# Optimization experiments

Hardware: AMD Instinct MI355X
Metric: run time of the kernel (lower is better)

Reference implementation:

```python
import jax, jax.numpy as jnp
import numpy as np

B, S, IN, OUT = 4, 2048, 4096, 4096


def setup_inputs() -> dict:
    key = jax.random.key(0)
    kx, kw, kb = jax.random.split(key, 3)
    x = jax.random.randint(kx, (B, S, IN), -127, 128, dtype=jnp.int8)
    weight = jax.random.randint(kw, (OUT, IN), -127, 128, dtype=jnp.int8)
    # original module initializes bias to zeros(int32); use random int32 to exercise the add
    bias = jax.random.randint(kb, (1, OUT), -1000, 1000, dtype=jnp.int32)
    return {"x": x, "weight": weight, "bias": bias}


def reference(x, weight, bias):
    x_shape = x.shape
    x2 = x.reshape(-1, x_shape[-1])  # [tokens, IN], int8
    # dot_general with preferred_element_type=int32 -> int8 inputs, int32 accumulate
    y = jax.lax.dot_general(
        x2, weight,
        dimension_numbers=(((1,), (1,)), ((), ())),
        preferred_element_type=jnp.int32,
    )  # [tokens, OUT] int32
    y = y + bias  # broadcast [1, OUT] int32
    return y.reshape(*x_shape[:-1], -1)
```

## Files before the change

kernel.cpp:

```cpp
#include <hip/hip_runtime.h>
#include <stdint.h>

#define M_TOT 8192
#define N_TOT 4096
#define K_TOT 4096

typedef int v4i  __attribute__((ext_vector_type(4)));
typedef int v16i __attribute__((ext_vector_type(16)));

__device__ __forceinline__ void gload_lds16(const void* g, void* l) {
    __builtin_amdgcn_global_load_lds(
        (const __attribute__((address_space(1))) unsigned int*)g,
        (__attribute__((address_space(3))) unsigned int*)l,
        16, 0, 0);
}

#define WAIT_VMCNT0() __builtin_amdgcn_s_waitcnt(0x0f70)

__global__ __launch_bounds__(256) void pack_i32_to_i8(
        const int4* __restrict__ src, int* __restrict__ dst, int n4) {
    int idx = blockIdx.x * 1024 + threadIdx.x;
#pragma unroll
    for (int u = 0; u < 4; ++u, idx += 256) {
        const int4 a = src[idx];
        dst[idx] = (a.x & 255) | ((a.y & 255) << 8) |
                   ((a.z & 255) << 16) | (a.w << 24);
    }
}

__global__ __launch_bounds__(256, 1) void i8gemm_bias(
        const signed char* __restrict__ x,
        const signed char* __restrict__ w,
        const int* __restrict__ bias,
        int* __restrict__ out) {
    __shared__ __align__(16) signed char la[2][256 * 64];
    __shared__ __align__(16) signed char lb[2][256 * 64];

    const int tid  = threadIdx.x;
    const int lane = tid & 63;
    const int wv   = tid >> 6;
    const int l31  = lane & 31;
    const int kh   = lane >> 5;
    const int wr   = wv >> 1;
    const int wc   = wv & 1;

    const int flat = blockIdx.y * gridDim.x + blockIdx.x;
    const int swz  = (flat & 7) * 64 + (flat >> 3);
    const int bn0  = (swz & 15) * 256;
    const int bm0  = (swz >> 4) * 256;

    int bv[4];
#pragma unroll
    for (int j = 0; j < 4; ++j) bv[j] = bias[bn0 + wc * 128 + j * 32 + l31];
    v16i acc[4][4];
#pragma unroll
    for (int i = 0; i < 4; ++i)
#pragma unroll
        for (int j = 0; j < 4; ++j)
#pragma unroll
            for (int r = 0; r < 16; ++r) acc[i][j][r] = bv[j];

    const int fc = (lane & 3) ^ ((lane >> 3) & 3);
    const signed char* pa = x + (long)(bm0 + wv * 64 + (lane >> 2)) * K_TOT + fc * 16;
    const signed char* pb = w + (long)(bn0 + wv * 64 + (lane >> 2)) * K_TOT + fc * 16;
    const int lbase = wv * 64 * 64;

    const int swr = (l31 >> 1) & 3;

#pragma unroll
    for (int i = 0; i < 4; ++i) {
        gload_lds16(pa + (long)i * 16 * K_TOT, &la[0][lbase + i * 1024]);
        gload_lds16(pb + (long)i * 16 * K_TOT, &lb[0][lbase + i * 1024]);
    }

    for (int kt = 0; kt < K_TOT / 64; ++kt) {
        const int cur = kt & 1;
        const signed char* lac = la[cur];
        const signed char* lbc = lb[cur];

        WAIT_VMCNT0();
        __builtin_amdgcn_s_barrier();
        __builtin_amdgcn_sched_barrier(0);

        v4i af[2][4], bf[2][4];
#pragma unroll
        for (int kk = 0; kk < 2; ++kk) {
            const int cs = ((kk * 2 + kh) ^ swr) * 16;
#pragma unroll
            for (int i = 0; i < 4; ++i) {
                af[kk][i] = *(const v4i*)(lac + (wr * 128 + i * 32 + l31) * 64 + cs);
                bf[kk][i] = *(const v4i*)(lbc + (wc * 128 + i * 32 + l31) * 64 + cs);
            }
        }
        __builtin_amdgcn_sched_barrier(0);

        if (kt + 1 < K_TOT / 64) {
            const long k0 = (long)(kt + 1) * 64;
            signed char* lan = la[cur ^ 1] + lbase;
            signed char* lbn = lb[cur ^ 1] + lbase;
#pragma unroll
            for (int i = 0; i < 4; ++i) {
                gload_lds16(pa + k0 + (long)i * 16 * K_TOT, lan + i * 1024);
                gload_lds16(pb + k0 + (long)i * 16 * K_TOT, lbn + i * 1024);
            }
        }
        __builtin_amdgcn_sched_barrier(0);

#pragma unroll
        for (int kk = 0; kk < 2; ++kk)
#pragma unroll
            for (int i = 0; i < 4; ++i)
#pragma unroll
                for (int j = 0; j < 4; ++j)
                    acc[i][j] = __builtin_amdgcn_mfma_i32_32x32x32_i8(
                        af[kk][i], bf[kk][j], acc[i][j], 0, 0, 0);
    }

#pragma unroll
    for (int i = 0; i < 4; ++i) {
        const int mbase = bm0 + wr * 128 + i * 32 + 4 * kh;
#pragma unroll
        for (int j = 0; j < 4; ++j) {
            const int n = bn0 + wc * 128 + j * 32 + l31;
#pragma unroll
            for (int r = 0; r < 16; ++r) {
                const int m = mbase + (r & 3) + 8 * (r >> 2);
                out[(long)m * N_TOT + n] = acc[i][j][r];
            }
        }
    }
}

extern "C" void kernel_launch(void* const* d_in, const int* in_sizes, int n_in,
                              void* d_out, int out_size, void* d_ws, size_t ws_size,
                              hipStream_t stream) {
    const int* x32  = (const int*)d_in[0];
    const int* w32  = (const int*)d_in[1];
    const int* bias = (const int*)d_in[2];
    int*       out  = (int*)d_out;

    signed char* xp = (signed char*)d_ws;
    signed char* wp = (signed char*)d_ws + (size_t)M_TOT * K_TOT;

    const int n4x = (M_TOT * K_TOT) / 4;
    const int n4w = (N_TOT * K_TOT) / 4;
    pack_i32_to_i8<<<n4x / 1024, 256, 0, stream>>>((const int4*)x32, (int*)xp, n4x);
    pack_i32_to_i8<<<n4w / 1024, 256, 0, stream>>>((const int4*)w32, (int*)wp, n4w);

    dim3 grid(N_TOT / 256, M_TOT / 256);
    i8gemm_bias<<<grid, 256, 0, stream>>>(xp, wp, bias, out);
}
```

Before: 418.0 us.

## Triple-buffer LDS tiles and prefetch two K-steps ahead in int8 GEMM

Replaces the double-buffered LDS pipeline with three rotating buffers per operand. Each iteration issues global-to-LDS loads for tile kt+2 and waits only until at most 8 loads are outstanding, instead of draining all of them. This gives global loads about a full extra iteration to arrive, so memory latency hides better behind the MFMA work. The cost is LDS growing from 64KB to 96KB and the pointer rotation adding some address arithmetic.

```diff
diff --git a/kernel.cpp b/kernel.cpp
--- a/kernel.cpp
+++ b/kernel.cpp
@@ -16,6 +16,7 @@
 }
 
 #define WAIT_VMCNT0() __builtin_amdgcn_s_waitcnt(0x0f70)
+#define WAIT_VMCNT8() __builtin_amdgcn_s_waitcnt(0x0f78)
 
 __global__ __launch_bounds__(256) void pack_i32_to_i8(
         const int4* __restrict__ src, int* __restrict__ dst, int n4) {
@@ -33,8 +34,8 @@
         const signed char* __restrict__ w,
         const int* __restrict__ bias,
         int* __restrict__ out) {
-    __shared__ __align__(16) signed char la[2][256 * 64];
-    __shared__ __align__(16) signed char lb[2][256 * 64];
+    __shared__ __align__(16) signed char la[3][256 * 64];
+    __shared__ __align__(16) signed char lb[3][256 * 64];
 
     const int tid  = threadIdx.x;
     const int lane = tid & 63;
@@ -67,19 +68,34 @@
 
     const int swr = (l31 >> 1) & 3;
 
+    signed char* A0 = &la[0][0]; signed char* A1 = &la[1][0]; signed char* A2 = &la[2][0];
+    signed char* B0 = &lb[0][0]; signed char* B1 = &lb[1][0]; signed char* B2 = &lb[2][0];
+
 #pragma unroll
     for (int i = 0; i < 4; ++i) {
-        gload_lds16(pa + (long)i * 16 * K_TOT, &la[0][lbase + i * 1024]);
-        gload_lds16(pb + (long)i * 16 * K_TOT, &lb[0][lbase + i * 1024]);
+        gload_lds16(pa + (long)i * 16 * K_TOT, A0 + lbase + i * 1024);
+        gload_lds16(pb + (long)i * 16 * K_TOT, B0 + lbase + i * 1024);
+    }
+#pragma unroll
+    for (int i = 0; i < 4; ++i) {
+        gload_lds16(pa + 64 + (long)i * 16 * K_TOT, A1 + lbase + i * 1024);
+        gload_lds16(pb + 64 + (long)i * 16 * K_TOT, B1 + lbase + i * 1024);
     }
 
-    for (int kt = 0; kt < K_TOT / 64; ++kt) {
-        const int cur = kt & 1;
-        const signed char* lac = la[cur];
-        const signed char* lbc = lb[cur];
+    const int NT = K_TOT / 64;
+    for (int kt = 0; kt < NT; ++kt) {
+        if (kt == NT - 1) { WAIT_VMCNT0(); } else { WAIT_VMCNT8(); }
+        __builtin_amdgcn_s_barrier();
+        __builtin_amdgcn_sched_barrier(0);
 
-        WAIT_VMCNT0();
-        __builtin_amdgcn_s_barrier();
+        if (kt + 2 < NT) {
+            const long k0 = (long)(kt + 2) * 64;
+#pragma unroll
+            for (int i = 0; i < 4; ++i) {
+                gload_lds16(pa + k0 + (long)i * 16 * K_TOT, A2 + lbase + i * 1024);
+                gload_lds16(pb + k0 + (long)i * 16 * K_TOT, B2 + lbase + i * 1024);
+            }
+        }
         __builtin_amdgcn_sched_barrier(0);
 
         v4i af[2][4], bf[2][4];
@@ -88,20 +104,8 @@
             const int cs = ((kk * 2 + kh) ^ swr) * 16;
 #pragma unroll
             for (int i = 0; i < 4; ++i) {
-                af[kk][i] = *(const v4i*)(lac + (wr * 128 + i * 32 + l31) * 64 + cs);
-                bf[kk][i] = *(const v4i*)(lbc + (wc * 128 + i * 32 + l31) * 64 + cs);
-            }
-        }
-        __builtin_amdgcn_sched_barrier(0);
-
-        if (kt + 1 < K_TOT / 64) {
-            const long k0 = (long)(kt + 1) * 64;
-            signed char* lan = la[cur ^ 1] + lbase;
-            signed char* lbn = lb[cur ^ 1] + lbase;
-#pragma unroll
-            for (int i = 0; i < 4; ++i) {
-                gload_lds16(pa + k0 + (long)i * 16 * K_TOT, lan + i * 1024);
-                gload_lds16(pb + k0 + (long)i * 16 * K_TOT, lbn + i * 1024);
+                af[kk][i] = *(const v4i*)(A0 + (wr * 128 + i * 32 + l31) * 64 + cs);
+                bf[kk][i] = *(const v4i*)(B0 + (wc * 128 + i * 32 + l31) * 64 + cs);
             }
         }
         __builtin_amdgcn_sched_barrier(0);
@@ -114,6 +118,10 @@
                 for (int j = 0; j < 4; ++j)
                     acc[i][j] = __builtin_amdgcn_mfma_i32_32x32x32_i8(
                         af[kk][i], bf[kk][j], acc[i][j], 0, 0, 0);
+
+        signed char* t;
+        t = A0; A0 = A1; A1 = A2; A2 = t;
+        t = B0; B0 = B1; B1 = B2; B2 = t;
     }
 
 #pragma unroll
```

Result: faster. 404.6 us (-3.2%).
